# Kernel tuning notes

Hardware: AMD Instinct MI355X
Metric: run time of the kernel (lower is better)

## Reference

```python
import jax, jax.numpy as jnp
import numpy as np

N_NODES = 50000
N_EDGES = 800000
IN_CH = 256
HID = 256
NUM_GRAPHS = 512
LEAKY_SLOPE = 0.01
EPS = 1e-5


def gcn_conv(x, src, dst, W, b):
    # src/dst already include self loops. Symmetric normalization D^-1/2 A_hat D^-1/2.
    deg = jnp.zeros((N_NODES,), x.dtype).at[dst].add(1.0)
    dinv = jax.lax.rsqrt(deg)  # deg >= 1 because of self loops
    norm = dinv[src] * dinv[dst]  # [E+N]
    h = x @ W  # [N, H] dense GEMM
    agg = jnp.zeros((N_NODES, W.shape[1]), x.dtype).at[dst].add(h[src] * norm[:, None])
    return agg + b


def layer_norm(x, w, b):
    mu = jnp.mean(x, axis=-1, keepdims=True)
    var = jnp.mean(jnp.square(x - mu), axis=-1, keepdims=True)
    return (x - mu) * jax.lax.rsqrt(var + EPS) * w + b


def setup_inputs() -> dict:
    key = jax.random.key(0)
    ks = jax.random.split(key, 8)
    x = jax.random.normal(ks[0], (N_NODES, IN_CH), dtype=jnp.float32)
    edge_index = jax.random.randint(ks[1], (2, N_EDGES), 0, N_NODES, dtype=jnp.int64)
    batch = jnp.sort(jax.random.randint(ks[2], (N_NODES,), 0, NUM_GRAPHS, dtype=jnp.int64))
    s1 = (2.0 / IN_CH) ** 0.5
    s2 = (2.0 / HID) ** 0.5
    W1 = jax.random.normal(ks[3], (IN_CH, HID), dtype=jnp.float32) * s1
    b1 = jnp.zeros((HID,), jnp.float32)
    W2 = jax.random.normal(ks[4], (HID, HID), dtype=jnp.float32) * s2
    b2 = jnp.zeros((HID,), jnp.float32)
    ln1_w = jnp.ones((HID,), jnp.float32)
    ln1_b = jnp.zeros((HID,), jnp.float32)
    ln2_w = jnp.ones((HID,), jnp.float32)
    ln2_b = jnp.zeros((HID,), jnp.float32)
    return {"x": x, "edge_index": edge_index, "batch": batch,
            "W1": W1, "b1": b1, "ln1_w": ln1_w, "ln1_b": ln1_b,
            "W2": W2, "b2": b2, "ln2_w": ln2_w, "ln2_b": ln2_b}


def reference(x, edge_index, batch, W1, b1, ln1_w, ln1_b, W2, b2, ln2_w, ln2_b):
    loop = jnp.arange(N_NODES, dtype=edge_index.dtype)
    src = jnp.concatenate([edge_index[0], loop])
    dst = jnp.concatenate([edge_index[1], loop])

    h = gcn_conv(x, src, dst, W1, b1)
    h = layer_norm(h, ln1_w, ln1_b)
    h = jnp.where(h >= 0, h, LEAKY_SLOPE * h)

    h = gcn_conv(h, src, dst, W2, b2)
    h = layer_norm(h, ln2_w, ln2_b)
    h = jnp.where(h >= 0, h, LEAKY_SLOPE * h)

    # global mean pool per graph (dropout is inference no-op)
    sums = jax.ops.segment_sum(h, batch, num_segments=NUM_GRAPHS)
    cnts = jax.ops.segment_sum(jnp.ones((N_NODES,), h.dtype), batch, num_segments=NUM_GRAPHS)
    return sums / jnp.maximum(cnts, 1.0)[:, None]
```

## Files before the change

### kernel.cpp

```cpp
#include <hip/hip_runtime.h>

#define N_NODES 50000
#define N_EDGES 800000
#define CH 256
#define NUM_GRAPHS 512
#define LEAKY 0.01f
#define LN_EPS 1e-5f
#define NBLK ((N_NODES + 255) / 256)

typedef __attribute__((ext_vector_type(4))) float f32x4;
typedef __attribute__((ext_vector_type(2))) float f32x2;
typedef __attribute__((ext_vector_type(8))) short bf16x8;

__device__ __forceinline__ float b2f(unsigned short u) {
    union { unsigned int i; float f; } x; x.i = ((unsigned int)u) << 16; return x.f;
}
__device__ __forceinline__ unsigned short f2b(float f) {
    union { float f; unsigned int i; } x; x.f = f;
    unsigned int r = x.i + 0x7fffu + ((x.i >> 16) & 1u);
    return (unsigned short)(r >> 16);
}
__device__ __forceinline__ f32x2 b2f2(unsigned int u) {
    union { unsigned int i; float f; } lo, hi;
    lo.i = u << 16; hi.i = u & 0xffff0000u;
    f32x2 r; r.x = lo.f; r.y = hi.f; return r;
}
__device__ __forceinline__ unsigned int pack2(float a, float b) {
    return (unsigned int)f2b(a) | ((unsigned int)f2b(b) << 16);
}
__device__ __forceinline__ void gload16(const void* g, void* l) {
    __builtin_amdgcn_global_load_lds((const __attribute__((address_space(1))) unsigned int*)g,
                                     (__attribute__((address_space(3))) unsigned int*)l, 16, 0, 0);
}

__global__ void prep(int* __restrict__ cnt,
                     const float* __restrict__ W1f, const float* __restrict__ W2f,
                     unsigned short* __restrict__ WT1, unsigned short* __restrict__ WT2) {
    int b = blockIdx.x;
    if (b < NBLK) {
        int i = b * 256 + threadIdx.x;
        if (i < N_NODES) cnt[i] = 0;
    } else {
        int bb = b - NBLK;
        int k = bb & 255;
        const float* W = (bb >> 8) ? W2f : W1f;
        unsigned short* WT = (bb >> 8) ? WT2 : WT1;
        WT[threadIdx.x * CH + k] = f2b(W[k * CH + threadIdx.x]);
    }
}

__global__ void count_deg(const int* __restrict__ dst, int* __restrict__ cnt) {
    int e = blockIdx.x * blockDim.x + threadIdx.x;
    if (e < N_EDGES) atomicAdd(&cnt[dst[e]], 1);
}

__global__ __launch_bounds__(256) void block_reduce(const int* __restrict__ cnt,
                                                    int* __restrict__ bsum,
                                                    float* __restrict__ dinv) {
    __shared__ int s[256];
    int tid = threadIdx.x;
    int i = blockIdx.x * 256 + tid;
    int v = (i < N_NODES) ? cnt[i] : 0;
    if (i < N_NODES) dinv[i] = rsqrtf(1.0f + (float)v);
    s[tid] = v;
    __syncthreads();
    #pragma unroll
    for (int off = 128; off > 0; off >>= 1) {
        if (tid < off) s[tid] += s[tid + off];
        __syncthreads();
    }
    if (tid == 0) bsum[blockIdx.x] = s[0];
}

__global__ __launch_bounds__(256) void block_scan(const int* __restrict__ cnt,
                                                  const int* __restrict__ bsum,
                                                  int* __restrict__ rowptr,
                                                  int* __restrict__ cursor) {
    __shared__ int s[256], sb[256];
    int tid = threadIdx.x;
    int i = blockIdx.x * 256 + tid;
    int bv = (tid < NBLK) ? bsum[tid] : 0;
    sb[tid] = bv;
    __syncthreads();
    #pragma unroll
    for (int off = 1; off < 256; off <<= 1) {
        int t = (tid >= off) ? sb[tid - off] : 0;
        __syncthreads();
        sb[tid] += t;
        __syncthreads();
    }
    const int base = (blockIdx.x == 0) ? 0 : sb[blockIdx.x - 1];
    int v = (i < N_NODES) ? cnt[i] : 0;
    s[tid] = v;
    __syncthreads();
    #pragma unroll
    for (int off = 1; off < 256; off <<= 1) {
        int t = (tid >= off) ? s[tid - off] : 0;
        __syncthreads();
        s[tid] += t;
        __syncthreads();
    }
    if (i < N_NODES) {
        int val = base + s[tid] - v;
        rowptr[i] = val;
        cursor[i] = val;
        if (i == N_NODES - 1) rowptr[N_NODES] = base + s[tid];
    }
}

__global__ void fill_csr(const int* __restrict__ src, const int* __restrict__ dst,
                         int* __restrict__ cursor, int* __restrict__ col) {
    int e = blockIdx.x * blockDim.x + threadIdx.x;
    if (e < N_EDGES) {
        int d = dst[e];
        int p = atomicAdd(&cursor[d], 1);
        col[p] = src[e];
    }
}

#define BM 128
#define SWZ2(r, c16) (((r) * 512 + (c16) * 16) ^ (((r) & 7) << 4))

__global__ __launch_bounds__(256) void gemm_bf16(const unsigned short* __restrict__ A,
                                                 const unsigned short* __restrict__ BT,
                                                 const float* __restrict__ dinv,
                                                 unsigned short* __restrict__ out) {
    __shared__ unsigned short As[BM * CH];
    const int row0 = blockIdx.x * BM;
    const int col0 = blockIdx.y * 128;
    const int tid = threadIdx.x;
    const int w = tid >> 6, l = tid & 63;
    const int wr = w >> 1, wc = w & 1;
    const int lr = l & 15, lg = l >> 4;

    {
        const int es = l >> 5, c16 = l & 31;
        #pragma unroll
        for (int it = 0; it < 16; it++) {
            const int r = it * 8 + w * 2 + es;
            const int kb = c16 ^ (r & 7);
            gload16(&A[(size_t)(row0 + r) * CH + kb * 8],
                    (char*)As + (it * 8 + w * 2) * 512);
        }
    }
    __syncthreads();

    f32x4 acc[4][4] = {};
    #pragma unroll
    for (int ks = 0; ks < 8; ks++) {
        bf16x8 af[4], bfr[4];
        #pragma unroll
        for (int fm = 0; fm < 4; fm++) {
            int r = wr * 64 + fm * 16 + lr;
            af[fm] = *(const bf16x8*)((const char*)As + SWZ2(r, ks * 4 + lg));
        }
        #pragma unroll
        for (int fn = 0; fn < 4; fn++) {
            bfr[fn] = *(const bf16x8*)&BT[(size_t)(col0 + wc * 64 + fn * 16 + lr) * CH + ks * 32 + lg * 8];
        }
        #pragma unroll
        for (int fm = 0; fm < 4; fm++)
            #pragma unroll
            for (int fn = 0; fn < 4; fn++)
                acc[fm][fn] = __builtin_amdgcn_mfma_f32_16x16x32_bf16(af[fm], bfr[fn], acc[fm][fn], 0, 0, 0);
    }

    #pragma unroll
    for (int fm = 0; fm < 4; fm++) {
        #pragma unroll
        for (int r = 0; r < 4; r++) {
            int grow = row0 + wr * 64 + fm * 16 + lg * 4 + r;
            if (grow < N_NODES) {
                float s = dinv[grow];
                #pragma unroll
                for (int fn = 0; fn < 4; fn++) {
                    int gcol = col0 + wc * 64 + fn * 16 + lr;
                    out[(size_t)grow * CH + gcol] = f2b(acc[fm][fn][r] * s);
                }
            }
        }
    }
}

__global__ __launch_bounds__(256) void gemm_f32a(const float* __restrict__ Af,
                                                 const unsigned short* __restrict__ BT,
                                                 const float* __restrict__ dinv,
                                                 unsigned short* __restrict__ out) {
    __shared__ unsigned short As[BM * CH];
    const int row0 = blockIdx.x * BM;
    const int col0 = blockIdx.y * 128;
    const int tid = threadIdx.x;
    const int w = tid >> 6, l = tid & 63;
    const int wr = w >> 1, wc = w & 1;
    const int lr = l & 15, lg = l >> 4;

    #pragma unroll
    for (int it = 0; it < 16; it++) {
        int cidx = it * 256 + tid;
        int r = cidx >> 5, kb = cidx & 31;
        int grow = row0 + r;
        uint4 ua = make_uint4(0u, 0u, 0u, 0u);
        if (grow < N_NODES) {
            const float* ap = &Af[(size_t)grow * CH + kb * 8];
            float4 v0 = *(const float4*)ap;
            float4 v1 = *(const float4*)(ap + 4);
            ua = make_uint4(pack2(v0.x, v0.y), pack2(v0.z, v0.w),
                            pack2(v1.x, v1.y), pack2(v1.z, v1.w));
        }
        *(uint4*)((char*)As + SWZ2(r, kb)) = ua;
    }
    __syncthreads();

    f32x4 acc[4][4] = {};
    #pragma unroll
    for (int ks = 0; ks < 8; ks++) {
        bf16x8 af[4], bfr[4];
        #pragma unroll
        for (int fm = 0; fm < 4; fm++) {
            int r = wr * 64 + fm * 16 + lr;
            af[fm] = *(const bf16x8*)((const char*)As + SWZ2(r, ks * 4 + lg));
        }
        #pragma unroll
        for (int fn = 0; fn < 4; fn++) {
            bfr[fn] = *(const bf16x8*)&BT[(size_t)(col0 + wc * 64 + fn * 16 + lr) * CH + ks * 32 + lg * 8];
        }
        #pragma unroll
        for (int fm = 0; fm < 4; fm++)
            #pragma unroll
            for (int fn = 0; fn < 4; fn++)
                acc[fm][fn] = __builtin_amdgcn_mfma_f32_16x16x32_bf16(af[fm], bfr[fn], acc[fm][fn], 0, 0, 0);
    }

    #pragma unroll
    for (int fm = 0; fm < 4; fm++) {
        #pragma unroll
        for (int r = 0; r < 4; r++) {
            int grow = row0 + wr * 64 + fm * 16 + lg * 4 + r;
            if (grow < N_NODES) {
                float s = dinv[grow];
                #pragma unroll
                for (int fn = 0; fn < 4; fn++) {
                    int gcol = col0 + wc * 64 + fn * 16 + lr;
                    out[(size_t)grow * CH + gcol] = f2b(acc[fm][fn][r] * s);
                }
            }
        }
    }
}

__global__ __launch_bounds__(256) void agg_ln_bf16(const unsigned short* __restrict__ h,
                                                   const int* __restrict__ rowptr,
                                                   const int* __restrict__ col,
                                                   const float* __restrict__ dinv,
                                                   const float* __restrict__ bias,
                                                   const float* __restrict__ lnw,
                                                   const float* __restrict__ lnb,
                                                   unsigned short* __restrict__ out) {
    const int w = threadIdx.x >> 6, lane = threadIdx.x & 63;
    const int d = blockIdx.x * 4 + w;
    if (d >= N_NODES) return;
    const int c4 = lane * 4;
    const uint2* __restrict__ h2 = (const uint2*)h;

    f32x2 acc01, acc23;
    {
        uint2 u = h2[(unsigned)(d * 64 + lane)];
        acc01 = b2f2(u.x); acc23 = b2f2(u.y);
    }

    const int e0 = rowptr[d], e1 = rowptr[d + 1];
    for (int base = e0; base < e1; base += 64) {
        int nch = e1 - base; if (nch > 64) nch = 64;
        int cidx = (lane < nch) ? col[base + lane] : 0;
        int j = 0;
        for (; j + 8 <= nch; j += 8) {
            int s0 = __shfl(cidx, j),     s1 = __shfl(cidx, j + 1);
            int s2 = __shfl(cidx, j + 2), s3 = __shfl(cidx, j + 3);
            int s4 = __shfl(cidx, j + 4), s5 = __shfl(cidx, j + 5);
            int s6 = __shfl(cidx, j + 6), s7 = __shfl(cidx, j + 7);
            uint2 u0 = h2[(unsigned)(s0 * 64 + lane)];
            uint2 u1 = h2[(unsigned)(s1 * 64 + lane)];
            uint2 u2 = h2[(unsigned)(s2 * 64 + lane)];
            uint2 u3 = h2[(unsigned)(s3 * 64 + lane)];
            uint2 u4 = h2[(unsigned)(s4 * 64 + lane)];
            uint2 u5 = h2[(unsigned)(s5 * 64 + lane)];
            uint2 u6 = h2[(unsigned)(s6 * 64 + lane)];
            uint2 u7 = h2[(unsigned)(s7 * 64 + lane)];
            acc01 += b2f2(u0.x) + b2f2(u1.x) + b2f2(u2.x) + b2f2(u3.x);
            acc23 += b2f2(u0.y) + b2f2(u1.y) + b2f2(u2.y) + b2f2(u3.y);
            acc01 += b2f2(u4.x) + b2f2(u5.x) + b2f2(u6.x) + b2f2(u7.x);
            acc23 += b2f2(u4.y) + b2f2(u5.y) + b2f2(u6.y) + b2f2(u7.y);
        }
        for (; j + 4 <= nch; j += 4) {
            int s0 = __shfl(cidx, j),     s1 = __shfl(cidx, j + 1);
            int s2 = __shfl(cidx, j + 2), s3 = __shfl(cidx, j + 3);
            uint2 u0 = h2[(unsigned)(s0 * 64 + lane)];
            uint2 u1 = h2[(unsigned)(s1 * 64 + lane)];
            uint2 u2 = h2[(unsigned)(s2 * 64 + lane)];
            uint2 u3 = h2[(unsigned)(s3 * 64 + lane)];
            acc01 += b2f2(u0.x) + b2f2(u1.x) + b2f2(u2.x) + b2f2(u3.x);
            acc23 += b2f2(u0.y) + b2f2(u1.y) + b2f2(u2.y) + b2f2(u3.y);
        }
        for (; j < nch; j++) {
            int s = __shfl(cidx, j);
            uint2 u = h2[(unsigned)(s * 64 + lane)];
            acc01 += b2f2(u.x); acc23 += b2f2(u.y);
        }
    }
    float a0 = acc01.x, a1 = acc01.y, a2 = acc23.x, a3 = acc23.y;
    const float di = dinv[d];
    float4 bb = *(const float4*)&bias[c4];
    a0 = a0 * di + bb.x; a1 = a1 * di + bb.y; a2 = a2 * di + bb.z; a3 = a3 * di + bb.w;

    float s1 = a0 + a1 + a2 + a3;
    float s2 = a0 * a0 + a1 * a1 + a2 * a2 + a3 * a3;
    #pragma unroll
    for (int off = 32; off > 0; off >>= 1) {
        s1 += __shfl_xor(s1, off);
        s2 += __shfl_xor(s2, off);
    }
    const float mu = s1 * (1.0f / CH);
    const float rstd = rsqrtf(s2 * (1.0f / CH) - mu * mu + LN_EPS);
    float4 wv = *(const float4*)&lnw[c4];
    float4 bv = *(const float4*)&lnb[c4];
    float y0 = (a0 - mu) * rstd * wv.x + bv.x;
    float y1 = (a1 - mu) * rstd * wv.y + bv.y;
    float y2 = (a2 - mu) * rstd * wv.z + bv.z;
    float y3 = (a3 - mu) * rstd * wv.w + bv.w;
    y0 = fmaxf(y0, LEAKY * y0);
    y1 = fmaxf(y1, LEAKY * y1);
    y2 = fmaxf(y2, LEAKY * y2);
    y3 = fmaxf(y3, LEAKY * y3);
    *(ushort4*)&out[(size_t)d * CH + c4] = make_ushort4(f2b(y0), f2b(y1), f2b(y2), f2b(y3));
}

__global__ __launch_bounds__(256) void pool_mean_bf16(const unsigned short* __restrict__ feat,
                                                      const int* __restrict__ batch,
                                                      float* __restrict__ out) {
    const int g = blockIdx.x;
    const int w = threadIdx.x >> 6, lane = threadIdx.x & 63;
    int lo = 0, hi = N_NODES;
    while (lo < hi) { int mid = (lo + hi) >> 1; if (batch[mid] < g) lo = mid + 1; else hi = mid; }
    const int start = lo;
    hi = N_NODES;
    while (lo < hi) { int mid = (lo + hi) >> 1; if (batch[mid] < g + 1) lo = mid + 1; else hi = mid; }
    const int end = lo;

    float a0 = 0.f, a1 = 0.f, a2 = 0.f, a3 = 0.f;
    for (int n = start + w; n < end; n += 4) {
        ushort4 u = *(const ushort4*)&feat[(size_t)n * CH + lane * 4];
        a0 += b2f(u.x); a1 += b2f(u.y); a2 += b2f(u.z); a3 += b2f(u.w);
    }
    __shared__ float4 red[4][64];
    red[w][lane] = make_float4(a0, a1, a2, a3);
    __syncthreads();
    if (w == 0) {
        float4 t0 = red[0][lane], t1 = red[1][lane], t2 = red[2][lane], t3 = red[3][lane];
        const float inv = (end > start) ? 1.0f / (float)(end - start) : 0.0f;
        float4 o = make_float4((t0.x + t1.x + t2.x + t3.x) * inv,
                               (t0.y + t1.y + t2.y + t3.y) * inv,
                               (t0.z + t1.z + t2.z + t3.z) * inv,
                               (t0.w + t1.w + t2.w + t3.w) * inv);
        *(float4*)&out[(size_t)g * CH + lane * 4] = o;
    }
}

static inline size_t align256(size_t x) { return (x + 255) & ~(size_t)255; }

extern "C" void kernel_launch(void* const* d_in, const int* in_sizes, int n_in,
                              void* d_out, int out_size, void* d_ws, size_t ws_size,
                              hipStream_t stream) {
    const float* x    = (const float*)d_in[0];
    const int*   edge = (const int*)d_in[1];
    const int*   batch= (const int*)d_in[2];
    const float* W1   = (const float*)d_in[3];
    const float* b1   = (const float*)d_in[4];
    const float* ln1w = (const float*)d_in[5];
    const float* ln1b = (const float*)d_in[6];
    const float* W2   = (const float*)d_in[7];
    const float* b2   = (const float*)d_in[8];
    const float* ln2w = (const float*)d_in[9];
    const float* ln2b = (const float*)d_in[10];

    const int* src = edge;
    const int* dst = edge + N_EDGES;

    char* p = (char*)d_ws;
    int* cnt    = (int*)p;  p += align256(N_NODES * 4);
    int* cursor = (int*)p;  p += align256(N_NODES * 4);
    int* rowptr = (int*)p;  p += align256((N_NODES + 1) * 4);
    int* bsum   = (int*)p;  p += align256(NBLK * 4);
    float* dinv = (float*)p; p += align256(N_NODES * 4);
    int* col    = (int*)p;  p += align256(N_EDGES * 4);
    unsigned short* wt1 = (unsigned short*)p; p += align256(CH * CH * 2);
    unsigned short* wt2 = (unsigned short*)p; p += align256(CH * CH * 2);
    unsigned short* bufA = (unsigned short*)p; p += align256((size_t)N_NODES * CH * 2);
    unsigned short* bufB = (unsigned short*)p; p += align256((size_t)N_NODES * CH * 2);
    p += 65536;

    prep<<<NBLK + 2 * CH, 256, 0, stream>>>(cnt, W1, W2, wt1, wt2);
    count_deg<<<(N_EDGES + 255) / 256, 256, 0, stream>>>(dst, cnt);
    block_reduce<<<NBLK, 256, 0, stream>>>(cnt, bsum, dinv);
    block_scan<<<NBLK, 256, 0, stream>>>(cnt, bsum, rowptr, cursor);
    fill_csr<<<(N_EDGES + 255) / 256, 256, 0, stream>>>(src, dst, cursor, col);

    dim3 ggrid((N_NODES + BM - 1) / BM, 2);
    gemm_f32a<<<ggrid, 256, 0, stream>>>(x, wt1, dinv, bufA);
    agg_ln_bf16<<<(N_NODES + 3) / 4, 256, 0, stream>>>(bufA, rowptr, col, dinv, b1, ln1w, ln1b, bufB);
    gemm_bf16<<<ggrid, 256, 0, stream>>>(bufB, wt2, dinv, bufA);
    agg_ln_bf16<<<(N_NODES + 3) / 4, 256, 0, stream>>>(bufA, rowptr, col, dinv, b2, ln2w, ln2b, bufB);
    pool_mean_bf16<<<NUM_GRAPHS, 256, 0, stream>>>(bufB, batch, (float*)d_out);
}
```

Measured before the change: 304.9 us.

## Split GEMM A-tile into per-wave K-chunked LDS buffers without block barriers

Both GEMM kernels stop loading the whole 128x256 A tile into shared memory behind a block-wide barrier. Each wave now stages only its own 64-row slice in K chunks of 64 into a private LDS buffer and synchronises with waitcnt instead of __syncthreads. This cuts LDS per block from 64KB to 32KB, which should allow more blocks per CU, and lets waves run independently. In exchange, two waves sharing the same rows now load the same A data twice, and the load of each chunk is not overlapped with that chunk's MFMAs.

```diff
diff --git a/kernel.cpp b/kernel.cpp
--- a/kernel.cpp
+++ b/kernel.cpp
@@ -119,62 +119,65 @@
 }
 
 #define BM 128
-#define SWZ2(r, c16) (((r) * 512 + (c16) * 16) ^ (((r) & 7) << 4))
+#define BN 128
+#define BK 64
+#define SWZ(row, kb) (((row) * 128 + (kb) * 16) ^ (((row) & 7) << 4))
 
 __global__ __launch_bounds__(256) void gemm_bf16(const unsigned short* __restrict__ A,
                                                  const unsigned short* __restrict__ BT,
                                                  const float* __restrict__ dinv,
                                                  unsigned short* __restrict__ out) {
-    __shared__ unsigned short As[BM * CH];
+    __shared__ unsigned short As[4][64 * 64];
     const int row0 = blockIdx.x * BM;
-    const int col0 = blockIdx.y * 128;
+    const int col0 = blockIdx.y * BN;
     const int tid = threadIdx.x;
     const int w = tid >> 6, l = tid & 63;
     const int wr = w >> 1, wc = w & 1;
     const int lr = l & 15, lg = l >> 4;
-
-    {
-        const int es = l >> 5, c16 = l & 31;
-        #pragma unroll
-        for (int it = 0; it < 16; it++) {
-            const int r = it * 8 + w * 2 + es;
-            const int kb = c16 ^ (r & 7);
-            gload16(&A[(size_t)(row0 + r) * CH + kb * 8],
-                    (char*)As + (it * 8 + w * 2) * 512);
-        }
-    }
-    __syncthreads();
+    const int sr = l >> 3, kbp = l & 7;
+    const int arow0 = row0 + wr * 64;
+    const int bcol0 = col0 + wc * 64;
+    unsigned short* myAs = As[w];
 
     f32x4 acc[4][4] = {};
-    #pragma unroll
-    for (int ks = 0; ks < 8; ks++) {
-        bf16x8 af[4], bfr[4];
-        #pragma unroll
-        for (int fm = 0; fm < 4; fm++) {
-            int r = wr * 64 + fm * 16 + lr;
-            af[fm] = *(const bf16x8*)((const char*)As + SWZ2(r, ks * 4 + lg));
-        }
-        #pragma unroll
-        for (int fn = 0; fn < 4; fn++) {
-            bfr[fn] = *(const bf16x8*)&BT[(size_t)(col0 + wc * 64 + fn * 16 + lr) * CH + ks * 32 + lg * 8];
-        }
-        #pragma unroll
-        for (int fm = 0; fm < 4; fm++)
+
+    for (int k0 = 0; k0 < CH; k0 += BK) {
+        asm volatile("s_waitcnt lgkmcnt(0)" ::: "memory");
+        #pragma unroll
+        for (int it = 0; it < 8; it++) {
+            const int R = it * 8;
+            const int r = R + sr;
+            const int kb = kbp ^ (r & 7);
+            gload16(&A[(size_t)(arow0 + r) * CH + k0 + kb * 8], (char*)myAs + R * 128);
+        }
+        asm volatile("s_waitcnt vmcnt(0)" ::: "memory");
+        __builtin_amdgcn_sched_barrier(0);
+        #pragma unroll
+        for (int ks = 0; ks < 2; ks++) {
+            bf16x8 af[4], bfr[4];
+            #pragma unroll
+            for (int fm = 0; fm < 4; fm++)
+                af[fm] = *(const bf16x8*)((const char*)myAs + SWZ(fm * 16 + lr, ks * 4 + lg));
             #pragma unroll
             for (int fn = 0; fn < 4; fn++)
-                acc[fm][fn] = __builtin_amdgcn_mfma_f32_16x16x32_bf16(af[fm], bfr[fn], acc[fm][fn], 0, 0, 0);
-    }
-
+                bfr[fn] = *(const bf16x8*)&BT[(size_t)(bcol0 + fn * 16 + lr) * CH + k0 + ks * 32 + lg * 8];
+            #pragma unroll
+            for (int fm = 0; fm < 4; fm++)
+                #pragma unroll
+                for (int fn = 0; fn < 4; fn++)
+                    acc[fm][fn] = __builtin_amdgcn_mfma_f32_16x16x32_bf16(af[fm], bfr[fn], acc[fm][fn], 0, 0, 0);
+        }
+    }
     #pragma unroll
     for (int fm = 0; fm < 4; fm++) {
         #pragma unroll
         for (int r = 0; r < 4; r++) {
-            int grow = row0 + wr * 64 + fm * 16 + lg * 4 + r;
+            int grow = arow0 + fm * 16 + lg * 4 + r;
             if (grow < N_NODES) {
                 float s = dinv[grow];
                 #pragma unroll
                 for (int fn = 0; fn < 4; fn++) {
-                    int gcol = col0 + wc * 64 + fn * 16 + lr;
+                    int gcol = bcol0 + fn * 16 + lr;
                     out[(size_t)grow * CH + gcol] = f2b(acc[fm][fn][r] * s);
                 }
             }
@@ -186,61 +189,61 @@
                                                  const unsigned short* __restrict__ BT,
                                                  const float* __restrict__ dinv,
                                                  unsigned short* __restrict__ out) {
-    __shared__ unsigned short As[BM * CH];
+    __shared__ unsigned short As[4][64 * 64];
     const int row0 = blockIdx.x * BM;
-    const int col0 = blockIdx.y * 128;
+    const int col0 = blockIdx.y * BN;
     const int tid = threadIdx.x;
     const int w = tid >> 6, l = tid & 63;
     const int wr = w >> 1, wc = w & 1;
     const int lr = l & 15, lg = l >> 4;
-
-    #pragma unroll
-    for (int it = 0; it < 16; it++) {
-        int cidx = it * 256 + tid;
-        int r = cidx >> 5, kb = cidx & 31;
-        int grow = row0 + r;
-        uint4 ua = make_uint4(0u, 0u, 0u, 0u);
-        if (grow < N_NODES) {
-            const float* ap = &Af[(size_t)grow * CH + kb * 8];
-            float4 v0 = *(const float4*)ap;
-            float4 v1 = *(const float4*)(ap + 4);
-            ua = make_uint4(pack2(v0.x, v0.y), pack2(v0.z, v0.w),
-                            pack2(v1.x, v1.y), pack2(v1.z, v1.w));
-        }
-        *(uint4*)((char*)As + SWZ2(r, kb)) = ua;
-    }
-    __syncthreads();
+    const int arow0 = row0 + wr * 64;
+    const int bcol0 = col0 + wc * 64;
+    unsigned short* myAs = As[w];
 
     f32x4 acc[4][4] = {};
-    #pragma unroll
-    for (int ks = 0; ks < 8; ks++) {
-        bf16x8 af[4], bfr[4];
-        #pragma unroll
-        for (int fm = 0; fm < 4; fm++) {
-            int r = wr * 64 + fm * 16 + lr;
-            af[fm] = *(const bf16x8*)((const char*)As + SWZ2(r, ks * 4 + lg));
-        }
-        #pragma unroll
-        for (int fn = 0; fn < 4; fn++) {
-            bfr[fn] = *(const bf16x8*)&BT[(size_t)(col0 + wc * 64 + fn * 16 + lr) * CH + ks * 32 + lg * 8];
-        }
-        #pragma unroll
-        for (int fm = 0; fm < 4; fm++)
+
+    for (int k0 = 0; k0 < CH; k0 += BK) {
+        #pragma unroll
+        for (int it = 0; it < 8; it++) {
+            int cidx = it * 64 + l;
+            int r = cidx >> 3, kb = cidx & 7;
+            int grow = arow0 + r;
+            uint4 ua = make_uint4(0u, 0u, 0u, 0u);
+            if (grow < N_NODES) {
+                const float* ap = &Af[(size_t)grow * CH + k0 + kb * 8];
+                float4 v0 = *(const float4*)ap;
+                float4 v1 = *(const float4*)(ap + 4);
+                ua = make_uint4(pack2(v0.x, v0.y), pack2(v0.z, v0.w),
+                                pack2(v1.x, v1.y), pack2(v1.z, v1.w));
+            }
+            *(uint4*)((char*)myAs + SWZ(r, kb)) = ua;
+        }
+        #pragma unroll
+        for (int ks = 0; ks < 2; ks++) {
+            bf16x8 af[4], bfr[4];
+            #pragma unroll
+            for (int fm = 0; fm < 4; fm++)
+                af[fm] = *(const bf16x8*)((const char*)myAs + SWZ(fm * 16 + lr, ks * 4 + lg));
             #pragma unroll
             for (int fn = 0; fn < 4; fn++)
-                acc[fm][fn] = __builtin_amdgcn_mfma_f32_16x16x32_bf16(af[fm], bfr[fn], acc[fm][fn], 0, 0, 0);
-    }
-
+                bfr[fn] = *(const bf16x8*)&BT[(size_t)(bcol0 + fn * 16 + lr) * CH + k0 + ks * 32 + lg * 8];
+            #pragma unroll
+            for (int fm = 0; fm < 4; fm++)
+                #pragma unroll
+                for (int fn = 0; fn < 4; fn++)
+                    acc[fm][fn] = __builtin_amdgcn_mfma_f32_16x16x32_bf16(af[fm], bfr[fn], acc[fm][fn], 0, 0, 0);
+        }
+    }
     #pragma unroll
     for (int fm = 0; fm < 4; fm++) {
         #pragma unroll
         for (int r = 0; r < 4; r++) {
-            int grow = row0 + wr * 64 + fm * 16 + lg * 4 + r;
+            int grow = arow0 + fm * 16 + lg * 4 + r;
             if (grow < N_NODES) {
                 float s = dinv[grow];
                 #pragma unroll
                 for (int fn = 0; fn < 4; fn++) {
-                    int gcol = col0 + wc * 64 + fn * 16 + lr;
+                    int gcol = bcol0 + fn * 16 + lr;
                     out[(size_t)grow * CH + gcol] = f2b(acc[fm][fn][r] * s);
                 }
             }
```

After: 309.4 us. About the same (+1.5%).
